# Optimization experiments

Measured on AMD Instinct MI355X. Metric: run time of the kernel, lower is better.

## Reference

```python
import jax, jax.numpy as jnp
import numpy as np

B, T, D_MODEL, D_HEAD = 4, 2048, 1024, 64

def setup_inputs() -> dict:
    key = jax.random.key(0)
    k1, k2, k3, k4 = jax.random.split(key, 4)
    x = jax.random.normal(k1, (B, T, D_MODEL), dtype=jnp.float32)
    # Linear(d_model, d_head) weights stored as [d_model, d_head] for x @ W
    s = 1.0 / np.sqrt(D_MODEL)
    W_Q = jax.random.normal(k2, (D_MODEL, D_HEAD), dtype=jnp.float32) * s
    W_K = jax.random.normal(k3, (D_MODEL, D_HEAD), dtype=jnp.float32) * s
    W_V = jax.random.normal(k4, (D_MODEL, D_HEAD), dtype=jnp.float32) * s
    return {"x": x, "W_Q": W_Q, "W_K": W_K, "W_V": W_V}

def reference(x, W_Q, W_K, W_V):
    d_head = W_Q.shape[-1]
    Q = jnp.einsum('btm,md->btd', x, W_Q)
    K = jnp.einsum('btm,md->btd', x, W_K)
    V = jnp.einsum('btm,md->btd', x, W_V)
    A = jnp.einsum('bid,bjd->bij', Q, K) / jnp.sqrt(jnp.asarray(d_head, x.dtype))
    T_ = x.shape[1]
    causal = jnp.tril(jnp.ones((T_, T_), dtype=bool))  # [T, T]
    A = jnp.where(causal, A, -jnp.inf)
    A = jax.nn.softmax(A, axis=-1)
    return jnp.einsum('bij,bjd->bid', A, V)
```

## Files before the change

### kernel.cpp

```cpp
#include <hip/hip_runtime.h>
#include <hip/hip_bf16.h>

#define NB 4
#define NT 2048
#define DM 1024
#define DH 64

typedef __attribute__((ext_vector_type(8))) short bf16x8;
typedef __attribute__((ext_vector_type(4))) float f32x4;
typedef unsigned short u16;
typedef unsigned int u32;

static __device__ __forceinline__ u16 f2b(float f) {
    __hip_bfloat16 h = __float2bfloat16(f);
    return __builtin_bit_cast(u16, h);
}
static __device__ __forceinline__ float b2f(u16 h) {
    return __builtin_bit_cast(float, (u32)h << 16);
}
static __device__ __forceinline__ void gld16(const void* g, void* l) {
    __builtin_amdgcn_global_load_lds((const __attribute__((address_space(1))) void*)g,
                                     (__attribute__((address_space(3))) void*)l, 16, 0, 0);
}
#define BAR() __builtin_amdgcn_s_barrier()
#define SBAR() __builtin_amdgcn_sched_barrier(0)

__global__ __launch_bounds__(256) void wt_conv(
    const float* __restrict__ WQ, const float* __restrict__ WK,
    const float* __restrict__ WV, u16* __restrict__ wt)
{
    __shared__ u16 tl[64][68];
    const int which = blockIdx.y, kt = blockIdx.x;
    const float* W = (which == 0) ? WQ : (which == 1) ? WK : WV;
    #pragma unroll
    for (int i = 0; i < 4; ++i) {
        int r = (threadIdx.x >> 4) + i * 16;
        int c = (threadIdx.x & 15) * 4;
        float4 v = *(const float4*)&W[(size_t)(kt * 64 + r) * DH + c];
        tl[r][c] = f2b(v.x); tl[r][c + 1] = f2b(v.y);
        tl[r][c + 2] = f2b(v.z); tl[r][c + 3] = f2b(v.w);
    }
    __syncthreads();
    int d = threadIdx.x >> 2, kc = (threadIdx.x & 3) * 16;
    u16 buf[16];
    #pragma unroll
    for (int j = 0; j < 16; ++j) buf[j] = tl[kc + j][d];
    u16* dst = wt + which * 65536 + d * 1024 + kt * 64 + kc;
    *(uint4*)dst = *(uint4*)&buf[0];
    *(uint4*)(dst + 8) = *(uint4*)&buf[8];
}

__global__ __launch_bounds__(256) void qkv_gemm(
    const float* __restrict__ x, const u16* __restrict__ wt,
    u16* __restrict__ Qb, u16* __restrict__ Kb, u16* __restrict__ Vt)
{
    __shared__ float xs[2][4096];
    __shared__ u16 wsm[2][4096];
    const int tid = threadIdx.x, lane = tid & 63, w = tid >> 6;
    const int l15 = lane & 15, g = lane >> 4;
    const int row0 = blockIdx.x * 64;
    const int which = blockIdx.y;
    const u16* Wg = wt + which * 65536;

    auto stage = [&](int kt, int bi) {
        #pragma unroll
        for (int i = 0; i < 4; ++i) {
            u32 D = (u32)(w * 4096 + i * 1024 + lane * 16);
            u32 r = D >> 8, c = D & 255;
            u32 cs = c ^ ((r & 7) << 5);
            gld16(x + (size_t)(row0 + r) * DM + kt * 64 + (cs >> 2),
                  (char*)&xs[bi][0] + w * 4096 + i * 1024);
        }
        #pragma unroll
        for (int i = 0; i < 2; ++i) {
            u32 D = (u32)(w * 2048 + i * 1024 + lane * 16);
            u32 r = D >> 7, c = D & 127;
            u32 cs = c ^ ((r & 7) << 4);
            gld16(Wg + (size_t)r * 1024 + kt * 64 + (cs >> 1),
                  (char*)&wsm[bi][0] + w * 2048 + i * 1024);
        }
    };

    f32x4 acc[4];
    #pragma unroll
    for (int i = 0; i < 4; ++i) acc[i] = {0.f, 0.f, 0.f, 0.f};

    stage(0, 0);

    const int arow = w * 16 + l15;
    #pragma unroll
    for (int kt = 0; kt < 16; ++kt) {
        if (kt < 15) {
            stage(kt + 1, (kt + 1) & 1);
            asm volatile("s_waitcnt vmcnt(6)" ::: "memory");
        } else {
            asm volatile("s_waitcnt vmcnt(0)" ::: "memory");
        }
        BAR();
        SBAR();
        const char* xb = (const char*)&xs[kt & 1][0];
        const char* wb = (const char*)&wsm[kt & 1][0];
        #pragma unroll
        for (int ks = 0; ks < 2; ++ks) {
            u32 abase = (u32)(arow * 256 + ks * 128 + g * 32);
            f32x4 a0 = *(const f32x4*)(xb + (abase ^ ((arow & 7) << 5)));
            f32x4 a1 = *(const f32x4*)(xb + ((abase + 16) ^ ((arow & 7) << 5)));
            bf16x8 afrag;
            #pragma unroll
            for (int e = 0; e < 4; ++e) afrag[e] = (short)f2b(a0[e]);
            #pragma unroll
            for (int e = 0; e < 4; ++e) afrag[4 + e] = (short)f2b(a1[e]);
            __builtin_amdgcn_s_setprio(1);
            #pragma unroll
            for (int nt = 0; nt < 4; ++nt) {
                int brow = nt * 16 + l15;
                u32 bb = (u32)(brow * 128 + ks * 64 + g * 16);
                bf16x8 bfrag = *(const bf16x8*)(wb + (bb ^ ((brow & 7) << 4)));
                acc[nt] = __builtin_amdgcn_mfma_f32_16x16x32_bf16(afrag, bfrag, acc[nt], 0, 0, 0);
            }
            __builtin_amdgcn_s_setprio(0);
        }
        BAR();
    }
    #pragma unroll
    for (int nt = 0; nt < 4; ++nt) {
        int dcol = nt * 16 + l15;
        #pragma unroll
        for (int r = 0; r < 4; ++r) {
            int row = row0 + w * 16 + g * 4 + r;
            float v = acc[nt][r];
            if (which == 0)      Qb[(size_t)row * DH + dcol] = f2b(v * 0.125f);
            else if (which == 1) Kb[(size_t)row * DH + dcol] = f2b(v);
            else { int bb2 = row >> 11, t = row & 2047;
                   Vt[(size_t)bb2 * DH * NT + (size_t)dcol * NT + t] = f2b(v); }
        }
    }
}

__global__ __launch_bounds__(256) void attn(
    const u16* __restrict__ Qb, const u16* __restrict__ Kb,
    const u16* __restrict__ Vt, u16* __restrict__ pOt, float* __restrict__ pml,
    int SLOTS)
{
    __shared__ u16 k_lds[2][4096];
    __shared__ u16 v_lds[2][4096];
    __shared__ f32x4 p_lds[4][128];

    const int tid = threadIdx.x, lane = tid & 63, w = tid >> 6;
    const int l15 = lane & 15, g = lane >> 4;
    const int b = blockIdx.y;

    int flat = blockIdx.x, qb = 0, nc;
    for (;;) { nc = (qb + 2) >> 1; if (flat < nc) break; flat -= nc; ++qb; }
    const int chunk = flat;
    const int t0 = chunk * 2;
    const int two = (t0 + 1 <= qb);
    const int q0 = qb * 64;

    const u16* Qg = Qb + ((size_t)b * NT + q0 + w * 16) * DH;
    const u16* Kg = Kb + (size_t)b * NT * DH;
    const u16* Vg = Vt + (size_t)b * DH * NT;

    bf16x8 qf[2];
    qf[0] = *(const bf16x8*)(Qg + l15 * DH + g * 8);
    qf[1] = *(const bf16x8*)(Qg + l15 * DH + 32 + g * 8);

    auto stage = [&](int t, int bi) {
        const int j0 = t * 64;
        #pragma unroll
        for (int i = 0; i < 2; ++i) {
            u32 D = (u32)(w * 2048 + i * 1024 + lane * 16);
            u32 r = D >> 7, c = D & 127;
            u32 cs = c ^ ((r & 7) << 4);
            gld16(Kg + (size_t)(j0 + r) * DH + (cs >> 1),
                  (char*)&k_lds[bi][0] + w * 2048 + i * 1024);
            gld16(Vg + (size_t)r * NT + j0 + (cs >> 1),
                  (char*)&v_lds[bi][0] + w * 2048 + i * 1024);
        }
    };
    stage(t0, 0);
    if (two) stage(t0 + 1, 1);

    float m_run = -INFINITY, l_run = 0.f;
    f32x4 oacc[4];
    #pragma unroll
    for (int nt = 0; nt < 4; ++nt) oacc[nt] = {0.f, 0.f, 0.f, 0.f};

    char* pw = (char*)&p_lds[w][0];
    const int swz = (l15 & 7) << 4;

    if (two) asm volatile("s_waitcnt vmcnt(4)" ::: "memory");
    else     asm volatile("s_waitcnt vmcnt(0)" ::: "memory");
    BAR();
    SBAR();

    #pragma unroll
    for (int ti = 0; ti < 2; ++ti) {
        if (ti == 1) {
            if (!two) break;
            asm volatile("s_waitcnt vmcnt(0)" ::: "memory");
            BAR();
            SBAR();
        }
        const int t = t0 + ti;
        const char* kb = (const char*)&k_lds[ti][0];
        const char* vb = (const char*)&v_lds[ti][0];

        f32x4 sacc[4];
        #pragma unroll
        for (int nt = 0; nt < 4; ++nt) sacc[nt] = {0.f, 0.f, 0.f, 0.f};
        __builtin_amdgcn_s_setprio(1);
        #pragma unroll
        for (int ks = 0; ks < 2; ++ks) {
            #pragma unroll
            for (int nt = 0; nt < 4; ++nt) {
                int arow = nt * 16 + l15;
                u32 aa = (u32)(arow * 128 + ks * 64 + g * 16);
                bf16x8 kf = *(const bf16x8*)(kb + (aa ^ ((arow & 7) << 4)));
                sacc[nt] = __builtin_amdgcn_mfma_f32_16x16x32_bf16(kf, qf[ks], sacc[nt], 0, 0, 0);
            }
        }
        __builtin_amdgcn_s_setprio(0);
        if (t == qb) {
            const int q_local = w * 16 + l15;
            #pragma unroll
            for (int nt = 0; nt < 4; ++nt)
                #pragma unroll
                for (int r = 0; r < 4; ++r)
                    if (nt * 16 + g * 4 + r > q_local) sacc[nt][r] = -1e30f;
        }
        float mx = -INFINITY;
        #pragma unroll
        for (int nt = 0; nt < 4; ++nt) {
            float a = fmaxf(fmaxf(sacc[nt][0], sacc[nt][1]),
                            fmaxf(sacc[nt][2], sacc[nt][3]));
            mx = fmaxf(mx, a);
        }
        mx = fmaxf(mx, __shfl_xor(mx, 16));
        mx = fmaxf(mx, __shfl_xor(mx, 32));
        const float m_new = fmaxf(m_run, mx);
        const float alpha = __expf(m_run - m_new);
        float p[4][4];
        float ps = 0.f;
        #pragma unroll
        for (int nt = 0; nt < 4; ++nt)
            #pragma unroll
            for (int r = 0; r < 4; ++r) {
                float pv = __expf(sacc[nt][r] - m_new);
                p[nt][r] = pv; ps += pv;
            }
        ps += __shfl_xor(ps, 16);
        ps += __shfl_xor(ps, 32);
        l_run = l_run * alpha + ps;
        m_run = m_new;
        #pragma unroll
        for (int nt = 0; nt < 4; ++nt)
            #pragma unroll
            for (int r = 0; r < 4; ++r) oacc[nt][r] *= alpha;

        #pragma unroll
        for (int nt = 0; nt < 4; ++nt) {
            uint2 pk;
            pk.x = (u32)f2b(p[nt][0]) | ((u32)f2b(p[nt][1]) << 16);
            pk.y = (u32)f2b(p[nt][2]) | ((u32)f2b(p[nt][3]) << 16);
            u32 a = (u32)((l15 * 128 + nt * 32 + g * 8) ^ swz);
            *(uint2*)(pw + a) = pk;
        }
        bf16x8 pb_[2];
        #pragma unroll
        for (int ks = 0; ks < 2; ++ks)
            pb_[ks] = *(const bf16x8*)(pw + ((u32)(l15 * 128 + ks * 64 + g * 16) ^ swz));

        __builtin_amdgcn_s_setprio(1);
        #pragma unroll
        for (int ks = 0; ks < 2; ++ks) {
            #pragma unroll
            for (int nt = 0; nt < 4; ++nt) {
                int arow = nt * 16 + l15;
                u32 aa = (u32)(arow * 128 + ks * 64 + g * 16);
                bf16x8 vf = *(const bf16x8*)(vb + (aa ^ ((arow & 7) << 4)));
                oacc[nt] = __builtin_amdgcn_mfma_f32_16x16x32_bf16(vf, pb_[ks], oacc[nt], 0, 0, 0);
            }
        }
        __builtin_amdgcn_s_setprio(0);
    }

    const int slot = (b * 32 + qb) * SLOTS + chunk;
    u16* Op = pOt + (size_t)slot * 4096;
    #pragma unroll
    for (int nt = 0; nt < 4; ++nt)
        #pragma unroll
        for (int r = 0; r < 4; ++r)
            Op[(nt * 16 + g * 4 + r) * 64 + w * 16 + l15] = f2b(oacc[nt][r]);
    if (g == 0) {
        float* mlp = pml + (size_t)slot * 128;
        mlp[(w * 16 + l15) * 2]     = m_run;
        mlp[(w * 16 + l15) * 2 + 1] = l_run;
    }
}

__global__ __launch_bounds__(256) void merge(
    const u16* __restrict__ pOt, const float* __restrict__ pml,
    float* __restrict__ out, int SLOTS)
{
    __shared__ float tl[64][65];
    const int bq = blockIdx.x;
    const int b = bq >> 5, qb = bq & 31;
    const int nc = (qb + 2) >> 1;
    const int base = bq * SLOTS;
    const int q = threadIdx.x & 63, ds = threadIdx.x >> 6;

    float m = -INFINITY;
    for (int c = 0; c < nc; ++c)
        m = fmaxf(m, pml[(size_t)(base + c) * 128 + q * 2]);
    float lsum = 0.f;
    float acc[16];
    #pragma unroll
    for (int i = 0; i < 16; ++i) acc[i] = 0.f;
    for (int c = 0; c < nc; ++c) {
        const float mc = pml[(size_t)(base + c) * 128 + q * 2];
        const float lc = pml[(size_t)(base + c) * 128 + q * 2 + 1];
        const float wc = __expf(mc - m);
        lsum += wc * lc;
        const u16* Op = pOt + (size_t)(base + c) * 4096;
        #pragma unroll
        for (int i = 0; i < 16; ++i)
            acc[i] += wc * b2f(Op[(ds * 16 + i) * 64 + q]);
    }
    const float inv = 1.f / lsum;
    #pragma unroll
    for (int i = 0; i < 16; ++i) tl[q][ds * 16 + i] = acc[i] * inv;
    __syncthreads();
    const int q2 = threadIdx.x >> 2, dc = threadIdx.x & 3;
    float* orow = out + ((size_t)b * NT + qb * 64 + q2) * 64 + dc * 16;
    #pragma unroll
    for (int j4 = 0; j4 < 4; ++j4) {
        float4 v = { tl[q2][dc * 16 + j4 * 4 + 0], tl[q2][dc * 16 + j4 * 4 + 1],
                     tl[q2][dc * 16 + j4 * 4 + 2], tl[q2][dc * 16 + j4 * 4 + 3] };
        *(float4*)&orow[j4 * 4] = v;
    }
}

extern "C" void kernel_launch(void* const* d_in, const int* in_sizes, int n_in,
                              void* d_out, int out_size, void* d_ws, size_t ws_size,
                              hipStream_t stream) {
    const float* x  = (const float*)d_in[0];
    const float* WQ = (const float*)d_in[1];
    const float* WK = (const float*)d_in[2];
    const float* WV = (const float*)d_in[3];
    float* out = (float*)d_out;

    char* ws = (char*)d_ws;
    u16* Qb = (u16*)ws;
    u16* Kb = (u16*)(ws + 1048576);
    u16* Vt = (u16*)(ws + 2097152);
    u16* Wt = (u16*)(ws + 3145728);
    const int SLOTS = 16;
    u16*   pOt = (u16*)(ws + 3538944);
    float* pml = (float*)(ws + 3538944 + (size_t)NB * 32 * SLOTS * 4096 * 2);

    wt_conv<<<dim3(16, 3), 256, 0, stream>>>(WQ, WK, WV, Wt);
    qkv_gemm<<<dim3(128, 3), 256, 0, stream>>>(x, Wt, Qb, Kb, Vt);
    attn<<<dim3(272, NB), 256, 0, stream>>>(Qb, Kb, Vt, pOt, pml, SLOTS);
    merge<<<NB * 32, 256, 0, stream>>>(pOt, pml, out, SLOTS);
}
```

Measured before the change: 46.60 us.

## Fuse attention and merge: split KV tiles across warps within a 16-query block

Replaces the split-KV attention kernel plus separate merge kernel with one kernel per 16-query block. Each of the four warps walks a strided subset of KV tiles, loading K and V fragments straight from global memory into registers instead of staging them through LDS. The four partial softmax states are then combined in shared memory and written as fp32 output. This drops a kernel launch and the bf16 partial-output round trip through global memory. In exchange, K/V reuse across query rows is lost, so global and L2 traffic for K/V rises, and warps within a block get unequal tile counts.

```diff
diff --git a/kernel.cpp b/kernel.cpp
--- a/kernel.cpp
+++ b/kernel.cpp
@@ -137,50 +137,31 @@
     }
 }
 
-__global__ __launch_bounds__(256) void attn(
+__global__ __launch_bounds__(256) void attn2(
     const u16* __restrict__ Qb, const u16* __restrict__ Kb,
-    const u16* __restrict__ Vt, u16* __restrict__ pOt, float* __restrict__ pml,
-    int SLOTS)
+    const u16* __restrict__ Vt, float* __restrict__ out)
 {
-    __shared__ u16 k_lds[2][4096];
-    __shared__ u16 v_lds[2][4096];
     __shared__ f32x4 p_lds[4][128];
+    __shared__ float o_lds[4][64][17];
+    __shared__ float ml_lds[4][2][16];
 
     const int tid = threadIdx.x, lane = tid & 63, w = tid >> 6;
     const int l15 = lane & 15, g = lane >> 4;
     const int b = blockIdx.y;
-
-    int flat = blockIdx.x, qb = 0, nc;
-    for (;;) { nc = (qb + 2) >> 1; if (flat < nc) break; flat -= nc; ++qb; }
-    const int chunk = flat;
-    const int t0 = chunk * 2;
-    const int two = (t0 + 1 <= qb);
-    const int q0 = qb * 64;
-
-    const u16* Qg = Qb + ((size_t)b * NT + q0 + w * 16) * DH;
-    const u16* Kg = Kb + (size_t)b * NT * DH;
-    const u16* Vg = Vt + (size_t)b * DH * NT;
+    const int qb16 = blockIdx.x;
+    const int q0 = qb16 * 16;
+    const int T = (qb16 >> 2) + 1;
+    const int tD = T - 1;
+    const int moff = (qb16 & 3) * 16;
+
+    const u16* Qg = Qb + ((size_t)b * NT + q0) * DH;
+    const u16* Kg = Kb + (size_t)b * NT * DH + (size_t)l15 * DH + g * 8;
+    const u16* Vg = Vt + (size_t)b * DH * NT + (size_t)l15 * NT + g * 8;
 
     bf16x8 qf[2];
     qf[0] = *(const bf16x8*)(Qg + l15 * DH + g * 8);
     qf[1] = *(const bf16x8*)(Qg + l15 * DH + 32 + g * 8);
 
-    auto stage = [&](int t, int bi) {
-        const int j0 = t * 64;
-        #pragma unroll
-        for (int i = 0; i < 2; ++i) {
-            u32 D = (u32)(w * 2048 + i * 1024 + lane * 16);
-            u32 r = D >> 7, c = D & 127;
-            u32 cs = c ^ ((r & 7) << 4);
-            gld16(Kg + (size_t)(j0 + r) * DH + (cs >> 1),
-                  (char*)&k_lds[bi][0] + w * 2048 + i * 1024);
-            gld16(Vg + (size_t)r * NT + j0 + (cs >> 1),
-                  (char*)&v_lds[bi][0] + w * 2048 + i * 1024);
-        }
-    };
-    stage(t0, 0);
-    if (two) stage(t0 + 1, 1);
-
     float m_run = -INFINITY, l_run = 0.f;
     f32x4 oacc[4];
     #pragma unroll
@@ -189,45 +170,39 @@
     char* pw = (char*)&p_lds[w][0];
     const int swz = (l15 & 7) << 4;
 
-    if (two) asm volatile("s_waitcnt vmcnt(4)" ::: "memory");
-    else     asm volatile("s_waitcnt vmcnt(0)" ::: "memory");
-    BAR();
-    SBAR();
-
-    #pragma unroll
-    for (int ti = 0; ti < 2; ++ti) {
-        if (ti == 1) {
-            if (!two) break;
-            asm volatile("s_waitcnt vmcnt(0)" ::: "memory");
-            BAR();
-            SBAR();
-        }
-        const int t = t0 + ti;
-        const char* kb = (const char*)&k_lds[ti][0];
-        const char* vb = (const char*)&v_lds[ti][0];
+    for (int t = w; t < T; t += 4) {
+        const int j0 = t * 64;
+        const u16* kp = Kg + (size_t)j0 * DH;
+        const u16* vp = Vg + j0;
+        bf16x8 kf[8], vf[8];
+        #pragma unroll
+        for (int nt = 0; nt < 4; ++nt) {
+            kf[nt * 2]     = *(const bf16x8*)(kp + nt * 16 * DH);
+            kf[nt * 2 + 1] = *(const bf16x8*)(kp + nt * 16 * DH + 32);
+        }
+        #pragma unroll
+        for (int nt = 0; nt < 4; ++nt) {
+            vf[nt * 2]     = *(const bf16x8*)(vp + nt * 16 * NT);
+            vf[nt * 2 + 1] = *(const bf16x8*)(vp + nt * 16 * NT + 32);
+        }
 
         f32x4 sacc[4];
         #pragma unroll
         for (int nt = 0; nt < 4; ++nt) sacc[nt] = {0.f, 0.f, 0.f, 0.f};
         __builtin_amdgcn_s_setprio(1);
         #pragma unroll
-        for (int ks = 0; ks < 2; ++ks) {
-            #pragma unroll
-            for (int nt = 0; nt < 4; ++nt) {
-                int arow = nt * 16 + l15;
-                u32 aa = (u32)(arow * 128 + ks * 64 + g * 16);
-                bf16x8 kf = *(const bf16x8*)(kb + (aa ^ ((arow & 7) << 4)));
-                sacc[nt] = __builtin_amdgcn_mfma_f32_16x16x32_bf16(kf, qf[ks], sacc[nt], 0, 0, 0);
-            }
-        }
+        for (int ks = 0; ks < 2; ++ks)
+            #pragma unroll
+            for (int nt = 0; nt < 4; ++nt)
+                sacc[nt] = __builtin_amdgcn_mfma_f32_16x16x32_bf16(
+                    kf[nt * 2 + ks], qf[ks], sacc[nt], 0, 0, 0);
         __builtin_amdgcn_s_setprio(0);
-        if (t == qb) {
-            const int q_local = w * 16 + l15;
+        if (t == tD) {
             #pragma unroll
             for (int nt = 0; nt < 4; ++nt)
                 #pragma unroll
                 for (int r = 0; r < 4; ++r)
-                    if (nt * 16 + g * 4 + r > q_local) sacc[nt][r] = -1e30f;
+                    if (nt * 16 + g * 4 + r > moff + l15) sacc[nt][r] = -1e30f;
         }
         float mx = -INFINITY;
         #pragma unroll
@@ -273,72 +248,44 @@
 
         __builtin_amdgcn_s_setprio(1);
         #pragma unroll
-        for (int ks = 0; ks < 2; ++ks) {
-            #pragma unroll
-            for (int nt = 0; nt < 4; ++nt) {
-                int arow = nt * 16 + l15;
-                u32 aa = (u32)(arow * 128 + ks * 64 + g * 16);
-                bf16x8 vf = *(const bf16x8*)(vb + (aa ^ ((arow & 7) << 4)));
-                oacc[nt] = __builtin_amdgcn_mfma_f32_16x16x32_bf16(vf, pb_[ks], oacc[nt], 0, 0, 0);
-            }
-        }
+        for (int ks = 0; ks < 2; ++ks)
+            #pragma unroll
+            for (int nt = 0; nt < 4; ++nt)
+                oacc[nt] = __builtin_amdgcn_mfma_f32_16x16x32_bf16(
+                    vf[nt * 2 + ks], pb_[ks], oacc[nt], 0, 0, 0);
         __builtin_amdgcn_s_setprio(0);
     }
 
-    const int slot = (b * 32 + qb) * SLOTS + chunk;
-    u16* Op = pOt + (size_t)slot * 4096;
+    if (g == 0) { ml_lds[w][0][l15] = m_run; ml_lds[w][1][l15] = l_run; }
     #pragma unroll
     for (int nt = 0; nt < 4; ++nt)
         #pragma unroll
         for (int r = 0; r < 4; ++r)
-            Op[(nt * 16 + g * 4 + r) * 64 + w * 16 + l15] = f2b(oacc[nt][r]);
-    if (g == 0) {
-        float* mlp = pml + (size_t)slot * 128;
-        mlp[(w * 16 + l15) * 2]     = m_run;
-        mlp[(w * 16 + l15) * 2 + 1] = l_run;
-    }
-}
-
-__global__ __launch_bounds__(256) void merge(
-    const u16* __restrict__ pOt, const float* __restrict__ pml,
-    float* __restrict__ out, int SLOTS)
-{
-    __shared__ float tl[64][65];
-    const int bq = blockIdx.x;
-    const int b = bq >> 5, qb = bq & 31;
-    const int nc = (qb + 2) >> 1;
-    const int base = bq * SLOTS;
-    const int q = threadIdx.x & 63, ds = threadIdx.x >> 6;
-
-    float m = -INFINITY;
-    for (int c = 0; c < nc; ++c)
-        m = fmaxf(m, pml[(size_t)(base + c) * 128 + q * 2]);
-    float lsum = 0.f;
-    float acc[16];
-    #pragma unroll
-    for (int i = 0; i < 16; ++i) acc[i] = 0.f;
-    for (int c = 0; c < nc; ++c) {
-        const float mc = pml[(size_t)(base + c) * 128 + q * 2];
-        const float lc = pml[(size_t)(base + c) * 128 + q * 2 + 1];
-        const float wc = __expf(mc - m);
-        lsum += wc * lc;
-        const u16* Op = pOt + (size_t)(base + c) * 4096;
-        #pragma unroll
-        for (int i = 0; i < 16; ++i)
-            acc[i] += wc * b2f(Op[(ds * 16 + i) * 64 + q]);
-    }
-    const float inv = 1.f / lsum;
-    #pragma unroll
-    for (int i = 0; i < 16; ++i) tl[q][ds * 16 + i] = acc[i] * inv;
+            o_lds[w][nt * 16 + g * 4 + r][l15] = oacc[nt][r];
     __syncthreads();
-    const int q2 = threadIdx.x >> 2, dc = threadIdx.x & 3;
-    float* orow = out + ((size_t)b * NT + qb * 64 + q2) * 64 + dc * 16;
-    #pragma unroll
-    for (int j4 = 0; j4 < 4; ++j4) {
-        float4 v = { tl[q2][dc * 16 + j4 * 4 + 0], tl[q2][dc * 16 + j4 * 4 + 1],
-                     tl[q2][dc * 16 + j4 * 4 + 2], tl[q2][dc * 16 + j4 * 4 + 3] };
-        *(float4*)&orow[j4 * 4] = v;
-    }
+
+    const int q = tid >> 4, d0 = (tid & 15) * 4;
+    float ms[4];
+    #pragma unroll
+    for (int s = 0; s < 4; ++s) ms[s] = ml_lds[s][0][q];
+    float mstar = fmaxf(fmaxf(ms[0], ms[1]), fmaxf(ms[2], ms[3]));
+    float wgt[4];
+    float L = 0.f;
+    #pragma unroll
+    for (int s = 0; s < 4; ++s) {
+        wgt[s] = __expf(ms[s] - mstar);
+        L += wgt[s] * ml_lds[s][1][q];
+    }
+    const float inv = 1.f / L;
+    float4 o;
+    #pragma unroll
+    for (int j = 0; j < 4; ++j) {
+        float v = 0.f;
+        #pragma unroll
+        for (int s = 0; s < 4; ++s) v += wgt[s] * o_lds[s][d0 + j][q];
+        (&o.x)[j] = v * inv;
+    }
+    *(float4*)&out[((size_t)b * NT + q0 + q) * DH + d0] = o;
 }
 
 extern "C" void kernel_launch(void* const* d_in, const int* in_sizes, int n_in,
@@ -355,12 +302,8 @@
     u16* Kb = (u16*)(ws + 1048576);
     u16* Vt = (u16*)(ws + 2097152);
     u16* Wt = (u16*)(ws + 3145728);
-    const int SLOTS = 16;
-    u16*   pOt = (u16*)(ws + 3538944);
-    float* pml = (float*)(ws + 3538944 + (size_t)NB * 32 * SLOTS * 4096 * 2);
 
     wt_conv<<<dim3(16, 3), 256, 0, stream>>>(WQ, WK, WV, Wt);
     qkv_gemm<<<dim3(128, 3), 256, 0, stream>>>(x, Wt, Qb, Kb, Vt);
-    attn<<<dim3(272, NB), 256, 0, stream>>>(Qb, Kb, Vt, pOt, pml, SLOTS);
-    merge<<<NB * 32, 256, 0, stream>>>(pOt, pml, out, SLOTS);
-}
+    attn2<<<dim3(NT / 16, NB), 256, 0, stream>>>(Qb, Kb, Vt, out);
+}
```

After: 57.39 us. 1.23x slower.
